# Kernel optimization log

Measured on AMD Instinct MI355X. Metric: run time of the kernel, lower is better.

Reference implementation:

```python
import jax, jax.numpy as jnp
import numpy as np

RES = 3.5
K = (np.pi / RES) ** 2          # Gaussian falloff constant
BW2 = 6.0                        # squared neighborhood radius (voxels)
R = 3                            # floor(idx - sqrt(6)) = idx-3, ceil(idx + sqrt(6)) = idx+3


def _offsets():
    o = jnp.arange(-R, R + 1)
    oz, oy, ox = jnp.meshgrid(o, o, o, indexing='ij')
    offs = jnp.stack([oz.ravel(), oy.ravel(), ox.ravel()], axis=-1)  # (343, 3)
    d2 = jnp.sum(offs * offs, axis=-1)                               # (343,)
    return offs, d2


def _splat(coords, x0, y0, z0, vox, G):
    """coords: (N,3) atom positions. Returns (G,G,G) density grid via scatter-max."""
    idx = jnp.stack([
        jnp.floor((coords[:, 0] - x0[0]) / vox[0]),
        jnp.floor((coords[:, 1] - y0[0]) / vox[0]),
        jnp.floor((coords[:, 2] - z0[0]) / vox[0]),
    ], axis=1).astype(jnp.int32)                                     # (N, 3)

    offs, d2 = _offsets()
    pos = idx[:, None, :] + offs[None, :, :]                         # (N, 343, 3)

    M = G - 1                                                        # min(dims) - 1 (cubic grid)
    lc = jnp.clip(idx - R, 0, M)                                     # clamped bbox lower (N,3)
    uc = jnp.clip(idx + R, 0, M)                                     # clamped bbox upper (N,3)
    in_range = jnp.all((pos >= lc[:, None, :]) & (pos <= uc[:, None, :]), axis=-1)
    center_ok = jnp.all((idx >= 0) & (idx < G), axis=-1)             # atom's own voxel inside grid
    valid = in_range & (d2 <= BW2)[None, :] & center_ok[:, None]     # (N, 343)

    prob = jnp.where(valid, jnp.exp(-K * d2.astype(jnp.float32))[None, :], 0.0)

    pos_c = jnp.clip(pos, 0, G - 1)                                  # safe indices for invalid slots
    flat = (pos_c[..., 0] * G + pos_c[..., 1]) * G + pos_c[..., 2]   # (N, 343)

    grid = jnp.zeros((G * G * G,), dtype=jnp.float32)
    grid = grid.at[flat.reshape(-1)].max(prob.reshape(-1))           # scatter-max (grid init 0, prob >= 0)
    return grid.reshape(G, G, G)


def setup_inputs() -> dict:
    key = jax.random.key(0)
    k1, k2 = jax.random.split(key)
    G = 256
    N = 20000
    src = jax.random.uniform(k1, (1, 3, N), dtype=jnp.float32, minval=0.0, maxval=float(G))
    tgt = jax.random.uniform(k2, (1, 3, N), dtype=jnp.float32, minval=0.0, maxval=float(G))
    return {
        'src': src,
        'tgt': tgt,
        'x_origin': jnp.zeros((1,), jnp.float32),
        'y_origin': jnp.zeros((1,), jnp.float32),
        'z_origin': jnp.zeros((1,), jnp.float32),
        'x_voxel': jnp.ones((1,), jnp.float32),
        'grid_dim': G,
    }


def reference(src, tgt, x_origin, y_origin, z_origin, x_voxel, grid_dim):
    G = int(grid_dim)
    src_c = src[0].T                                                 # (N, 3)
    tgt_c = tgt[0].T
    src_mask = _splat(src_c, x_origin, y_origin, z_origin, x_voxel, G)
    tgt_mask = _splat(tgt_c, x_origin, y_origin, z_origin, x_voxel, G)
    # global_alignment_loss: tgt <- tgt*src ; src <- src*src ; loss = mean(sum(src) - sum(tgt))
    rho_em = jnp.sum(tgt_mask * src_mask)
    rho_mo = jnp.sum(src_mask * src_mask)
    return rho_mo - rho_em
```

## Files before the change

### kernel.cpp

```cpp
#include <hip/hip_runtime.h>

#define GDIM   256
#define TDIM   32
#define NTILE  8
#define NTILES 512
#define CAP    160
#define NQ     4096

__constant__ int2 OFF01[21] = {
    {-2,-1},{-2,0},{-2,1},
    {-1,-2},{-1,-1},{-1,0},{-1,1},{-1,2},
    { 0,-2},{ 0,-1},{ 0,0},{ 0,1},{ 0,2},
    { 1,-2},{ 1,-1},{ 1,0},{ 1,1},{ 1,2},
    { 2,-1},{ 2,0},{ 2,1},
};
__constant__ unsigned long long PAT01[21] = {
    0x0040204000ull, 0x0020102000ull, 0x0040204000ull,
    0x0040204000ull, 0x4008040840ull, 0x2004020420ull, 0x4008040840ull, 0x0040204000ull,
    0x0020102000ull, 0x2004020420ull, 0x1002010210ull, 0x2004020420ull, 0x0020102000ull,
    0x0040204000ull, 0x4008040840ull, 0x2004020420ull, 0x4008040840ull, 0x0040204000ull,
    0x0040204000ull, 0x0020102000ull, 0x0040204000ull,
};

__global__ void bin_kernel(const float* __restrict__ src,
                           const float* __restrict__ tgt,
                           const float* __restrict__ ox,
                           const float* __restrict__ oy,
                           const float* __restrict__ oz,
                           const float* __restrict__ vox,
                           unsigned* __restrict__ cnt,
                           unsigned* __restrict__ entries,
                           int N)
{
    int tid = blockIdx.x * blockDim.x + threadIdx.x;
    if (tid >= 2 * N) return;
    int a = tid % N;
    int m = tid / N;

    const float* c = m ? tgt : src;
    float vx = vox[0];
    int i0 = (int)floorf((c[a]         - ox[0]) / vx);
    int i1 = (int)floorf((c[N + a]     - oy[0]) / vx);
    int i2 = (int)floorf((c[2 * N + a] - oz[0]) / vx);
    if ((unsigned)i0 >= GDIM || (unsigned)i1 >= GDIM || (unsigned)i2 >= GDIM) return;

    unsigned pk = (unsigned)i0 | ((unsigned)i1 << 8) | ((unsigned)i2 << 16);
    int tl0 = max(i0 - 2, 0) >> 5, th0 = min(i0 + 2, GDIM - 1) >> 5;
    int tl1 = max(i1 - 2, 0) >> 5, th1 = min(i1 + 2, GDIM - 1) >> 5;
    int tl2 = max(i2 - 2, 0) >> 5, th2 = min(i2 + 2, GDIM - 1) >> 5;

    for (int t0 = tl0; t0 <= th0; ++t0)
        for (int t1 = tl1; t1 <= th1; ++t1)
            for (int t2 = tl2; t2 <= th2; ++t2) {
                int bin = m * NTILES + ((t0 * NTILE + t1) * NTILE + t2);
                unsigned slot = atomicAdd(&cnt[bin], 1u);
                if (slot < CAP) entries[bin * CAP + slot] = pk;
            }
}

__global__ __launch_bounds__(256)
void tile_kernel(const unsigned* __restrict__ cnt,
                 const unsigned* __restrict__ entries,
                 float* __restrict__ out)
{
    __shared__ unsigned long long smem[2 * NQ];
    __shared__ float tbl[8];
    __shared__ float wsum[4];

    int tid = threadIdx.x;
    int t   = blockIdx.x;
    int tx0 = ((t >> 6) & 7) << 5;
    int ty0 = ((t >> 3) & 7) << 5;
    int tz0 = (t & 7) << 5;

    if (tid < 8) {
        const float kf = (float)((3.14159265358979323846 / 3.5) * (3.14159265358979323846 / 3.5));
        tbl[tid] = (tid < 7) ? expf(-kf * (float)tid) : 0.0f;
    }
    {
        uint4* zp = (uint4*)smem;
        for (int i = tid; i < 4096; i += 256) zp[i] = make_uint4(0u, 0u, 0u, 0u);
    }
    int nS = min(cnt[t],          (unsigned)CAP);
    int nT = min(cnt[NTILES + t], (unsigned)CAP);
    __syncthreads();

    int totS = nS * 21;
    int tot  = totS + nT * 21;
    for (int task = tid; task < tot; task += 256) {
        int m  = task >= totS;
        int lt = m ? task - totS : task;
        int e  = lt / 21, r = lt % 21;
        unsigned pk = entries[(m * NTILES + t) * CAP + e];
        int i0 = pk & 255, i1 = (pk >> 8) & 255, i2 = (pk >> 16) & 255;
        int2 o = OFF01[r];
        int l0 = i0 + o.x - tx0; if ((unsigned)l0 >= TDIM) continue;
        int l1 = i1 + o.y - ty0; if ((unsigned)l1 >= TDIM) continue;
        int zs = max(i2 - 2, tz0), ze = min(i2 + 2, tz0 + TDIM - 1);
        int drop = zs - (i2 - 2), keep = ze - zs + 1;
        unsigned long long pat =
            (PAT01[r] >> (8 * drop)) & ((1ull << (8 * keep)) - 1ull);
        if (!pat) continue;
        int lb  = (l0 << 10) | (l1 << 5) | (zs - tz0);
        int off = lb & 7;
        unsigned long long* q = &smem[m * NQ + (lb >> 3)];
        unsigned long long lo = pat << (8 * off);
        if (lo) atomicOr(q, lo);
        if (off + keep > 8) {
            unsigned long long hi = pat >> (8 * (8 - off));
            if (hi) atomicOr(q + 1, hi);
        }
    }
    __syncthreads();

    float acc = 0.0f;
    const ulonglong2* sp = (const ulonglong2*)smem;
    const ulonglong2* tp = (const ulonglong2*)(smem + NQ);
    for (int i = tid; i < NQ / 2; i += 256) {
        ulonglong2 s = sp[i];
        if ((s.x | s.y) == 0ull) continue;
        ulonglong2 tv = tp[i];
        unsigned long long sv[2] = {s.x, s.y};
        unsigned long long tw[2] = {tv.x, tv.y};
        #pragma unroll
        for (int k = 0; k < 2; ++k) {
            unsigned long long sw = sv[k];
            unsigned long long twv = tw[k];
            while (sw) {
                int bit  = __ffsll((long long)sw) - 1;
                int byte = bit >> 3;
                float vs = tbl[bit & 7];
                unsigned tb = (unsigned)((twv >> (byte << 3)) & 0xffull);
                float vt = tbl[__ffs((int)(tb | 0x80u)) - 1];
                acc += vs * (vs - vt);
                sw &= ~(0xffull << (byte << 3));
            }
        }
    }
    #pragma unroll
    for (int off2 = 32; off2 > 0; off2 >>= 1)
        acc += __shfl_down(acc, off2, 64);
    int lane = tid & 63, wv = tid >> 6;
    if (lane == 0) wsum[wv] = acc;
    __syncthreads();
    if (tid == 0)
        atomicAdd(out, wsum[0] + wsum[1] + wsum[2] + wsum[3]);
}

extern "C" void kernel_launch(void* const* d_in, const int* in_sizes, int n_in,
                              void* d_out, int out_size, void* d_ws, size_t ws_size,
                              hipStream_t stream)
{
    const float* src = (const float*)d_in[0];
    const float* tgt = (const float*)d_in[1];
    const float* ox  = (const float*)d_in[2];
    const float* oy  = (const float*)d_in[3];
    const float* oz  = (const float*)d_in[4];
    const float* vox = (const float*)d_in[5];
    int N = in_sizes[0] / 3;

    unsigned* cnt     = (unsigned*)d_ws;
    unsigned* entries = cnt + 2 * NTILES;

    hipMemsetAsync(cnt, 0, 2 * NTILES * sizeof(unsigned), stream);
    hipMemsetAsync(d_out, 0, sizeof(float), stream);

    int nb = (2 * N + 255) / 256;
    bin_kernel<<<nb, 256, 0, stream>>>(src, tgt, ox, oy, oz, vox, cnt, entries, N);
    tile_kernel<<<NTILES, 256, 0, stream>>>(cnt, entries, (float*)d_out);
}
```

Baseline: 99.88 us.

## Use 16x16x64 column tiles, stage entries in LDS, fold output zeroing into binning

Tiles change from 32^3 cubes (512 blocks) to 16x16x64 columns (1024 blocks), and the per-bin capacity shrinks to match. This doubles parallelism on the many-CU GPU and halves the LDS used per block, which should allow more resident blocks. Each block now copies its entry list into shared memory once, so the 21 tasks per entry no longer re-read it from global memory. The output memset is dropped and the bin kernel zeroes the output instead. In exchange, atoms near tile edges are duplicated into more bins, and a bin that overflows the smaller CAP would silently drop atoms.

```diff
diff --git a/kernel.cpp b/kernel.cpp
--- a/kernel.cpp
+++ b/kernel.cpp
@@ -1,11 +1,9 @@
 #include <hip/hip_runtime.h>
 
 #define GDIM   256
-#define TDIM   32
-#define NTILE  8
-#define NTILES 512
-#define CAP    160
-#define NQ     4096
+#define NCOLS  1024
+#define CAP    128
+#define NQ     2048
 
 __constant__ int2 OFF01[21] = {
     {-2,-1},{-2,0},{-2,1},
@@ -30,9 +28,11 @@
                            const float* __restrict__ vox,
                            unsigned* __restrict__ cnt,
                            unsigned* __restrict__ entries,
+                           float* __restrict__ out,
                            int N)
 {
     int tid = blockIdx.x * blockDim.x + threadIdx.x;
+    if (tid == 0) *out = 0.0f;
     if (tid >= 2 * N) return;
     int a = tid % N;
     int m = tid / N;
@@ -45,14 +45,14 @@
     if ((unsigned)i0 >= GDIM || (unsigned)i1 >= GDIM || (unsigned)i2 >= GDIM) return;
 
     unsigned pk = (unsigned)i0 | ((unsigned)i1 << 8) | ((unsigned)i2 << 16);
-    int tl0 = max(i0 - 2, 0) >> 5, th0 = min(i0 + 2, GDIM - 1) >> 5;
-    int tl1 = max(i1 - 2, 0) >> 5, th1 = min(i1 + 2, GDIM - 1) >> 5;
-    int tl2 = max(i2 - 2, 0) >> 5, th2 = min(i2 + 2, GDIM - 1) >> 5;
+    int tlx = max(i0 - 2, 0) >> 4, thx = min(i0 + 2, GDIM - 1) >> 4;
+    int tly = max(i1 - 2, 0) >> 4, thy = min(i1 + 2, GDIM - 1) >> 4;
+    int tlz = max(i2 - 2, 0) >> 6, thz = min(i2 + 2, GDIM - 1) >> 6;
 
-    for (int t0 = tl0; t0 <= th0; ++t0)
-        for (int t1 = tl1; t1 <= th1; ++t1)
-            for (int t2 = tl2; t2 <= th2; ++t2) {
-                int bin = m * NTILES + ((t0 * NTILE + t1) * NTILE + t2);
+    for (int tx = tlx; tx <= thx; ++tx)
+        for (int ty = tly; ty <= thy; ++ty)
+            for (int tz = tlz; tz <= thz; ++tz) {
+                int bin = m * NCOLS + (((tx << 4) + ty) << 2) + tz;
                 unsigned slot = atomicAdd(&cnt[bin], 1u);
                 if (slot < CAP) entries[bin * CAP + slot] = pk;
             }
@@ -64,14 +64,15 @@
                  float* __restrict__ out)
 {
     __shared__ unsigned long long smem[2 * NQ];
+    __shared__ unsigned eS[CAP], eT[CAP];
     __shared__ float tbl[8];
     __shared__ float wsum[4];
 
     int tid = threadIdx.x;
     int t   = blockIdx.x;
-    int tx0 = ((t >> 6) & 7) << 5;
-    int ty0 = ((t >> 3) & 7) << 5;
-    int tz0 = (t & 7) << 5;
+    int cx0 = (t >> 6) << 4;
+    int cy0 = ((t >> 2) & 15) << 4;
+    int cz0 = (t & 3) << 6;
 
     if (tid < 8) {
         const float kf = (float)((3.14159265358979323846 / 3.5) * (3.14159265358979323846 / 3.5));
@@ -79,10 +80,12 @@
     }
     {
         uint4* zp = (uint4*)smem;
-        for (int i = tid; i < 4096; i += 256) zp[i] = make_uint4(0u, 0u, 0u, 0u);
+        for (int i = tid; i < 2048; i += 256) zp[i] = make_uint4(0u, 0u, 0u, 0u);
     }
-    int nS = min(cnt[t],          (unsigned)CAP);
-    int nT = min(cnt[NTILES + t], (unsigned)CAP);
+    int nS = min(cnt[t],         (unsigned)CAP);
+    int nT = min(cnt[NCOLS + t], (unsigned)CAP);
+    for (int i = tid; i < nS; i += 256) eS[i] = entries[t * CAP + i];
+    for (int i = tid; i < nT; i += 256) eT[i] = entries[(NCOLS + t) * CAP + i];
     __syncthreads();
 
     int totS = nS * 21;
@@ -91,17 +94,17 @@
         int m  = task >= totS;
         int lt = m ? task - totS : task;
         int e  = lt / 21, r = lt % 21;
-        unsigned pk = entries[(m * NTILES + t) * CAP + e];
+        unsigned pk = m ? eT[e] : eS[e];
         int i0 = pk & 255, i1 = (pk >> 8) & 255, i2 = (pk >> 16) & 255;
         int2 o = OFF01[r];
-        int l0 = i0 + o.x - tx0; if ((unsigned)l0 >= TDIM) continue;
-        int l1 = i1 + o.y - ty0; if ((unsigned)l1 >= TDIM) continue;
-        int zs = max(i2 - 2, tz0), ze = min(i2 + 2, tz0 + TDIM - 1);
+        int l0 = i0 + o.x - cx0; if ((unsigned)l0 >= 16) continue;
+        int l1 = i1 + o.y - cy0; if ((unsigned)l1 >= 16) continue;
+        int zs = max(i2 - 2, cz0), ze = min(i2 + 2, cz0 + 63);
         int drop = zs - (i2 - 2), keep = ze - zs + 1;
         unsigned long long pat =
             (PAT01[r] >> (8 * drop)) & ((1ull << (8 * keep)) - 1ull);
         if (!pat) continue;
-        int lb  = (l0 << 10) | (l1 << 5) | (zs - tz0);
+        int lb  = (l0 << 10) | (l1 << 6) | (zs - cz0);
         int off = lb & 7;
         unsigned long long* q = &smem[m * NQ + (lb >> 3)];
         unsigned long long lo = pat << (8 * off);
@@ -124,7 +127,7 @@
         unsigned long long tw[2] = {tv.x, tv.y};
         #pragma unroll
         for (int k = 0; k < 2; ++k) {
-            unsigned long long sw = sv[k];
+            unsigned long long sw  = sv[k];
             unsigned long long twv = tw[k];
             while (sw) {
                 int bit  = __ffsll((long long)sw) - 1;
@@ -160,12 +163,12 @@
     int N = in_sizes[0] / 3;
 
     unsigned* cnt     = (unsigned*)d_ws;
-    unsigned* entries = cnt + 2 * NTILES;
+    unsigned* entries = cnt + 2 * NCOLS;
 
-    hipMemsetAsync(cnt, 0, 2 * NTILES * sizeof(unsigned), stream);
-    hipMemsetAsync(d_out, 0, sizeof(float), stream);
+    hipMemsetAsync(cnt, 0, 2 * NCOLS * sizeof(unsigned), stream);
 
     int nb = (2 * N + 255) / 256;
-    bin_kernel<<<nb, 256, 0, stream>>>(src, tgt, ox, oy, oz, vox, cnt, entries, N);
-    tile_kernel<<<NTILES, 256, 0, stream>>>(cnt, entries, (float*)d_out);
+    bin_kernel<<<nb, 256, 0, stream>>>(src, tgt, ox, oy, oz, vox, cnt, entries,
+                                       (float*)d_out, N);
+    tile_kernel<<<NCOLS, 256, 0, stream>>>(cnt, entries, (float*)d_out);
 }
```

After: 96.09 us. -3.8%, faster.
